# Kernel tuning notes

Hardware: AMD Instinct MI355X
Metric: run time of the kernel (lower is better)

Reference implementation:

```python
import jax, jax.numpy as jnp
import numpy as np

B, N = 4, 2048
INPUT_DIM, KDIM, VDIM = 128, 128, 16
EMBED, V_EMBED, H = 128, 128, 8
HEAD_DIM = EMBED // H          # 16
V_HEAD_DIM = V_EMBED // H      # 16 (== VDIM, required by the torch view)
SCALING = HEAD_DIM ** -0.5


def setup_inputs() -> dict:
    key = jax.random.key(0)
    ks = jax.random.split(key, 12)
    inp = {
        "query": jax.random.normal(ks[0], (B, N, INPUT_DIM), dtype=jnp.float32),
        "key": jax.random.normal(ks[1], (B, N, KDIM), dtype=jnp.float32),
        "value": jax.random.normal(ks[2], (B, N, VDIM), dtype=jnp.float32),
        # nn.Linear weights are [out, in]; init.normal_ -> std normal
        "Wq": jax.random.normal(ks[3], (EMBED, INPUT_DIM), dtype=jnp.float32),
        "bq": jnp.zeros((EMBED,), dtype=jnp.float32),
        "Wk": jax.random.normal(ks[4], (EMBED, KDIM), dtype=jnp.float32),
        "bk": jnp.zeros((EMBED,), dtype=jnp.float32),
        "Wv": jax.random.normal(ks[5], (V_EMBED, VDIM), dtype=jnp.float32),
        "bv": jnp.zeros((V_EMBED,), dtype=jnp.float32),
        "Wo": jax.random.normal(ks[6], (V_EMBED // H, V_EMBED), dtype=jnp.float32),
        "bo": jnp.zeros((V_EMBED // H,), dtype=jnp.float32),
    }
    return inp


def reference(query, key, value, Wq, bq, Wk, bk, Wv, bv, Wo, bo):
    # projections
    q = (query @ Wq.T + bq) * SCALING                 # [B, N, EMBED]
    k = key @ Wk.T + bk                               # [B, N, EMBED]
    v = value @ Wv.T + bv                             # [B, N, V_EMBED]
    # split heads: [B, H, N, head_dim]
    q = q.reshape(B, N, H, HEAD_DIM).transpose(0, 2, 1, 3)
    k = k.reshape(B, N, H, HEAD_DIM).transpose(0, 2, 1, 3)
    v = v.reshape(B, N, H, V_HEAD_DIM).transpose(0, 2, 1, 3)
    # full NxN scores (naive attention, as in the source)
    scores = jnp.einsum("bhnd,bhmd->bhnm", q, k)      # [B, H, N, N]
    attn = jax.nn.softmax(scores, axis=-1)
    # dropout is identity in eval mode
    ctx = jnp.einsum("bhnm,bhme->bhne", attn, v)      # [B, H, N, V_HEAD_DIM]
    ctx = ctx.transpose(0, 2, 1, 3).reshape(B, N, V_EMBED)
    out = ctx @ Wo.T + bo                             # [B, N, V_EMBED // H]
    return out
```

## Files before the change

kernel.cpp:

```cpp
#include <hip/hip_runtime.h>
#include <math.h>

typedef unsigned short ushort_t;
typedef unsigned int uint_t;
typedef __bf16 bf16x8 __attribute__((ext_vector_type(8)));
typedef float f32x4 __attribute__((ext_vector_type(4)));

#define NSEQ 2048
#define BH   32
#define QSCALE 0.3606737602222409f

__device__ __forceinline__ float exp2_fast(float x) {
#if __has_builtin(__builtin_amdgcn_exp2f)
    return __builtin_amdgcn_exp2f(x);
#else
    return exp2f(x);
#endif
}

__device__ __forceinline__ ushort_t f2bf(float x) {
    uint_t u = __float_as_uint(x);
    u += 0x7FFFu + ((u >> 16) & 1u);
    return (ushort_t)(u >> 16);
}
__device__ __forceinline__ float bf2f(ushort_t h) {
    return __uint_as_float(((uint_t)h) << 16);
}
__device__ __forceinline__ uint_t pkbf(float a, float b) {
    return ((__float_as_uint(a) + 0x8000u) >> 16) |
           ((__float_as_uint(b) + 0x8000u) & 0xFFFF0000u);
}

union U8 { ushort_t u[8]; bf16x8 v; uint4 q; };
union F8 { float f[8]; float4 v4[2]; };

__global__ __launch_bounds__(256) void wpack_kernel(
    const float* __restrict__ Wq, const float* __restrict__ Wk,
    ushort_t* __restrict__ wpk_hi, ushort_t* __restrict__ wpk_lo)
{
    const int idx  = blockIdx.x * 256 + threadIdx.x;
    const int lane = idx & 63;
    const int f    = (idx >> 6) & 3;
    const int ct   = (idx >> 8) & 7;
    const int mat  = idx >> 11;
    const float* W = mat ? Wk : Wq;
    const float* src = W + (size_t)(ct * 16 + (lane & 15)) * 128
                         + f * 32 + (lane >> 4) * 8;
    F8 x; x.v4[0] = *(const float4*)src; x.v4[1] = *(const float4*)(src + 4);
    U8 hi, lo;
#pragma unroll
    for (int j = 0; j < 8; ++j) {
        const ushort_t h = f2bf(x.f[j]);
        hi.u[j] = h;
        lo.u[j] = f2bf(x.f[j] - bf2f(h));
    }
    const size_t dst = (size_t)mat * 16384 + ((size_t)(ct * 4 + f) * 64 + lane) * 8;
    *(uint4*)(wpk_hi + dst) = hi.q;
    *(uint4*)(wpk_lo + dst) = lo.q;
}

__global__ __launch_bounds__(256, 2) void proj_kernel(
    const float* __restrict__ query, const float* __restrict__ key,
    const float* __restrict__ value,
    const float* __restrict__ bq, const float* __restrict__ bk,
    const float* __restrict__ Wv, const float* __restrict__ bv,
    const ushort_t* __restrict__ wpk_hi, const ushort_t* __restrict__ wpk_lo,
    ushort_t* __restrict__ q_hi, ushort_t* __restrict__ q_lo,
    ushort_t* __restrict__ k_hi, ushort_t* __restrict__ k_lo,
    ushort_t* __restrict__ vt)
{
    const int t   = threadIdx.x;
    const int w   = t >> 6;
    const int l   = t & 63;
    const int n16 = l & 15;
    const int g   = l >> 4;
    const int rbase = blockIdx.x * 16;
    const int b = rbase >> 11;

    const int isK    = w >> 1;
    const int cthalf = (w & 1) * 4;

    const float* X = isK ? key : query;
    const float* xrow = X + (size_t)(rbase + n16) * 128 + g * 8;
    bf16x8 ah[4], al[4];
#pragma unroll
    for (int f = 0; f < 4; ++f) {
        F8 x;
        x.v4[0] = *(const float4*)(xrow + f * 32);
        x.v4[1] = *(const float4*)(xrow + f * 32 + 4);
        U8 hi, lo;
#pragma unroll
        for (int j = 0; j < 8; ++j) {
            const ushort_t h = f2bf(x.f[j]);
            hi.u[j] = h;
            lo.u[j] = f2bf(x.f[j] - bf2f(h));
        }
        ah[f] = hi.v; al[f] = lo.v;
    }

    bf16x8 bhfr[4][4], blfr[4][4];
#pragma unroll
    for (int ctl = 0; ctl < 4; ++ctl) {
#pragma unroll
        for (int f = 0; f < 4; ++f) {
            const size_t o = (size_t)isK * 16384
                           + ((size_t)((cthalf + ctl) * 4 + f) * 64 + l) * 8;
            bhfr[ctl][f] = *(const bf16x8*)(wpk_hi + o);
            blfr[ctl][f] = *(const bf16x8*)(wpk_lo + o);
        }
    }

    const float* bias = isK ? bk : bq;
    ushort_t* dhi = isK ? k_hi : q_hi;
    ushort_t* dlo = isK ? k_lo : q_lo;
    const float scale = isK ? 1.0f : QSCALE;
    const int nbase = (rbase & 2047) + g * 4;

#pragma unroll
    for (int ctl = 0; ctl < 4; ++ctl) {
        const int h = cthalf + ctl;
        const float bval = bias[h * 16 + n16];
        f32x4 acc = {bval, bval, bval, bval};
#pragma unroll
        for (int f = 0; f < 4; ++f) {
            acc = __builtin_amdgcn_mfma_f32_16x16x32_bf16(ah[f], bhfr[ctl][f], acc, 0, 0, 0);
            acc = __builtin_amdgcn_mfma_f32_16x16x32_bf16(al[f], bhfr[ctl][f], acc, 0, 0, 0);
            acc = __builtin_amdgcn_mfma_f32_16x16x32_bf16(ah[f], blfr[ctl][f], acc, 0, 0, 0);
        }
        const size_t abase = ((size_t)(b * 8 + h) * NSEQ + nbase) * 16 + n16;
#pragma unroll
        for (int r = 0; r < 3 + 1; ++r) {
            const float vq = acc[r] * scale;
            const ushort_t hh = f2bf(vq);
            dhi[abase + (size_t)r * 16] = hh;
            dlo[abase + (size_t)r * 16] = f2bf(vq - bf2f(hh));
        }
    }

    const int e  = t & 127;
    const int rh = t >> 7;
    const int r0 = rbase + rh * 8;
    const float4* Wv4 = (const float4*)(Wv + (size_t)e * 16);
    const float4 wv0 = Wv4[0], wv1 = Wv4[1], wv2 = Wv4[2], wv3 = Wv4[3];
    const float bvv = bv[e];
    U8 vpk;
#pragma unroll
    for (int r = 0; r < 8; ++r) {
        const float4* xv4 = (const float4*)(value + (size_t)(r0 + r) * 16);
        const float4 x0 = xv4[0], x1 = xv4[1], x2 = xv4[2], x3 = xv4[3];
        float a = bvv;
        a += wv0.x*x0.x + wv0.y*x0.y + wv0.z*x0.z + wv0.w*x0.w;
        a += wv1.x*x1.x + wv1.y*x1.y + wv1.z*x1.z + wv1.w*x1.w;
        a += wv2.x*x2.x + wv2.y*x2.y + wv2.z*x2.z + wv2.w*x2.w;
        a += wv3.x*x3.x + wv3.y*x3.y + wv3.z*x3.z + wv3.w*x3.w;
        vpk.u[r] = f2bf(a);
    }
    const int hv = e >> 4, dd = e & 15;
    *(uint4*)(vt + ((size_t)(b * 8 + hv) * 16 + dd) * NSEQ + (r0 & 2047)) = vpk.q;
}

__global__ __launch_bounds__(256) void attn_kernel(
    const ushort_t* __restrict__ q_hi, const ushort_t* __restrict__ q_lo,
    const ushort_t* __restrict__ k_hi, const ushort_t* __restrict__ k_lo,
    const ushort_t* __restrict__ vt, float* __restrict__ ctx)
{
    const int t    = threadIdx.x;
    const int wave = t >> 6;
    const int l    = t & 63;
    const int col  = l & 15;
    const int g    = l >> 4;

    const int bh = blockIdx.y;
    const int qb = blockIdx.x * 64 + wave * 16;

    __shared__ __align__(16) ushort_t lds_p[4][16 * 40];
    ushort_t* pbuf = lds_p[wave];

    U8 Uz, Uo;
#pragma unroll
    for (int i = 0; i < 8; ++i) { Uz.u[i] = 0; Uo.u[i] = 0x3F80; }
    const bf16x8 zf = Uz.v, ones = Uo.v;

    const size_t qoff = ((size_t)(bh * NSEQ + qb + col)) * 16 + (g & 1) * 8;
    const bf16x8 bq1 = *(const bf16x8*)(q_hi + qoff);
    bf16x8 bq2 = *(const bf16x8*)(q_lo + qoff);
    bq2 = (g < 2) ? bq2 : zf;

    const ushort_t* ksel = (g < 2) ? k_hi : k_lo;
    const ushort_t* aptr = ksel + ((size_t)(bh * NSEQ + col)) * 16 + (g & 1) * 8;
    const ushort_t* vptr = vt + ((size_t)(bh * 16 + col)) * NSEQ + g * 8;

    f32x4 o    = {0.f, 0.f, 0.f, 0.f};
    f32x4 lacc = {0.f, 0.f, 0.f, 0.f};
    float m_run = -INFINITY;

    bf16x8 a1 = *(const bf16x8*)(aptr);
    bf16x8 a2 = *(const bf16x8*)(aptr + 256);
    bf16x8 av = *(const bf16x8*)(vptr);

    for (int kb = 0; kb < 64; ++kb) {
        const int kn = (kb + 1) & 63;
        bf16x8 na1 = *(const bf16x8*)(aptr + (size_t)kn * 512);
        bf16x8 na2 = *(const bf16x8*)(aptr + (size_t)kn * 512 + 256);
        bf16x8 nav = *(const bf16x8*)(vptr + (size_t)kn * 32);

        f32x4 z = {0.f, 0.f, 0.f, 0.f};
        f32x4 st1 = __builtin_amdgcn_mfma_f32_16x16x32_bf16(a1, bq2, z, 0, 0, 0);
        st1       = __builtin_amdgcn_mfma_f32_16x16x32_bf16(a1, bq1, st1, 0, 0, 0);
        f32x4 st2 = __builtin_amdgcn_mfma_f32_16x16x32_bf16(a2, bq2, z, 0, 0, 0);
        st2       = __builtin_amdgcn_mfma_f32_16x16x32_bf16(a2, bq1, st2, 0, 0, 0);

        float tm = fmaxf(fmaxf(fmaxf(st1[0], st1[1]), fmaxf(st1[2], st1[3])),
                         fmaxf(fmaxf(st2[0], st2[1]), fmaxf(st2[2], st2[3])));
        tm = fmaxf(tm, __shfl_xor(tm, 16));
        tm = fmaxf(tm, __shfl_xor(tm, 32));

        const float m_new = fmaxf(m_run, tm);
        const float alpha = exp2_fast(m_run - m_new);
        m_run = m_new;

        float p0 = exp2_fast(st1[0] - m_new);
        float p1 = exp2_fast(st1[1] - m_new);
        float p2 = exp2_fast(st1[2] - m_new);
        float p3 = exp2_fast(st1[3] - m_new);
        float p4 = exp2_fast(st2[0] - m_new);
        float p5 = exp2_fast(st2[1] - m_new);
        float p6 = exp2_fast(st2[2] - m_new);
        float p7 = exp2_fast(st2[3] - m_new);

        o[0] *= alpha; o[1] *= alpha; o[2] *= alpha; o[3] *= alpha;
        lacc[0] *= alpha; lacc[1] *= alpha; lacc[2] *= alpha; lacc[3] *= alpha;

        uint2 w1; w1.x = pkbf(p0, p1); w1.y = pkbf(p2, p3);
        uint2 w2; w2.x = pkbf(p4, p5); w2.y = pkbf(p6, p7);
        *(uint2*)(pbuf + col * 40 + 4 * g)      = w1;
        *(uint2*)(pbuf + col * 40 + 16 + 4 * g) = w2;
        const bf16x8 bp = *(const bf16x8*)(pbuf + col * 40 + 8 * g);

        o    = __builtin_amdgcn_mfma_f32_16x16x32_bf16(av,   bp, o,    0, 0, 0);
        lacc = __builtin_amdgcn_mfma_f32_16x16x32_bf16(ones, bp, lacc, 0, 0, 0);

        a1 = na1; a2 = na2; av = nav;
    }

    const float linv = 1.0f / lacc[0];
    f32x4 res;
    res[0] = o[0] * linv; res[1] = o[1] * linv;
    res[2] = o[2] * linv; res[3] = o[3] * linv;
    *(f32x4*)(ctx + ((size_t)(bh * NSEQ + qb + col)) * 16 + 4 * g) = res;
}

__global__ __launch_bounds__(256) void outproj_kernel(
    const float* __restrict__ ctxws, const float* __restrict__ Wo,
    const float* __restrict__ bo, float* __restrict__ out)
{
    __shared__ float wo_s[16 * 132];
    const int t = threadIdx.x;
    for (int i = t; i < 2048; i += 256) {
        const int j = i >> 7, e2 = i & 127;
        wo_s[j * 132 + e2] = Wo[i];
    }
    __syncthreads();

    const int rl = t >> 4, j = t & 15;
    const int row = blockIdx.x * 16 + rl;
    const int b = row >> 11, n = row & 2047;
    float acc = bo[j];
#pragma unroll
    for (int h = 0; h < 8; ++h) {
        const float4* cp4 = (const float4*)(ctxws + (((size_t)(b*8 + h) * NSEQ) + n) * 16);
#pragma unroll
        for (int d4 = 0; d4 < 4; ++d4) {
            const float4 cc = cp4[d4];
            const float* wp = &wo_s[j * 132 + h * 16 + d4 * 4];
            acc += cc.x*wp[0] + cc.y*wp[1] + cc.z*wp[2] + cc.w*wp[3];
        }
    }
    out[(size_t)row * 16 + j] = acc;
}

extern "C" void kernel_launch(void* const* d_in, const int* in_sizes, int n_in,
                              void* d_out, int out_size, void* d_ws, size_t ws_size,
                              hipStream_t stream)
{
    const float* query = (const float*)d_in[0];
    const float* key_  = (const float*)d_in[1];
    const float* value = (const float*)d_in[2];
    const float* Wq = (const float*)d_in[3];
    const float* bq = (const float*)d_in[4];
    const float* Wk = (const float*)d_in[5];
    const float* bk = (const float*)d_in[6];
    const float* Wv = (const float*)d_in[7];
    const float* bv = (const float*)d_in[8];
    const float* Wo = (const float*)d_in[9];
    const float* bo = (const float*)d_in[10];
    float* out = (float*)d_out;

    ushort_t* q_hi = (ushort_t*)d_ws;
    ushort_t* q_lo = q_hi + (1u << 20);
    ushort_t* k_hi = q_hi + (2u << 20);
    ushort_t* k_lo = q_hi + (3u << 20);
    ushort_t* vt   = q_hi + (4u << 20);
    float*    ctx  = (float*)((char*)d_ws + (10u << 20));
    ushort_t* wpk_hi = (ushort_t*)((char*)d_ws + (14u << 20));
    ushort_t* wpk_lo = wpk_hi + 32768;

    wpack_kernel<<<dim3(16), dim3(256), 0, stream>>>(Wq, Wk, wpk_hi, wpk_lo);
    proj_kernel<<<dim3(512), dim3(256), 0, stream>>>(
        query, key_, value, bq, bk, Wv, bv, wpk_hi, wpk_lo,
        q_hi, q_lo, k_hi, k_lo, vt);
    attn_kernel<<<dim3(32, 32), dim3(256), 0, stream>>>(
        q_hi, q_lo, k_hi, k_lo, vt, ctx);
    outproj_kernel<<<dim3(512), dim3(256), 0, stream>>>(ctx, Wo, bo, out);
}
```

Baseline: 146.3 us.

## Precompute row max in separate pass to drop online softmax rescaling

Adds a maxk_kernel that computes an approximate per-query row max (hi-only Q times K hi+lo) in a first pass. The attention kernel then folds -max into the MFMA accumulator init, which removes the per-block max reduction, the cross-lane shuffles and the alpha rescaling of the output and normalizer. Float-to-bf16 packing also switches to the packed hardware conversion intrinsic, and the projection weight fragments are loaded per iteration to lower register pressure. The cost is an extra full pass over K plus a kernel launch, and an approximate max that could allow slight overflow or underflow risk.

```diff
diff --git a/kernel.cpp b/kernel.cpp
--- a/kernel.cpp
+++ b/kernel.cpp
@@ -1,4 +1,5 @@
 #include <hip/hip_runtime.h>
+#include <hip/hip_bf16.h>
 #include <math.h>
 
 typedef unsigned short ushort_t;
@@ -18,21 +19,25 @@
 #endif
 }
 
-__device__ __forceinline__ ushort_t f2bf(float x) {
-    uint_t u = __float_as_uint(x);
-    u += 0x7FFFu + ((u >> 16) & 1u);
-    return (ushort_t)(u >> 16);
-}
-__device__ __forceinline__ float bf2f(ushort_t h) {
-    return __uint_as_float(((uint_t)h) << 16);
-}
-__device__ __forceinline__ uint_t pkbf(float a, float b) {
-    return ((__float_as_uint(a) + 0x8000u) >> 16) |
-           ((__float_as_uint(b) + 0x8000u) & 0xFFFF0000u);
-}
-
-union U8 { ushort_t u[8]; bf16x8 v; uint4 q; };
+union U8 { ushort_t u[8]; bf16x8 v; uint4 q; uint_t w[4]; };
 union F8 { float f[8]; float4 v4[2]; };
+
+__device__ __forceinline__ uint_t pk2(float a, float b) {
+    __hip_bfloat162 h2 = __float22bfloat162_rn(make_float2(a, b));
+    union { __hip_bfloat162 h; uint_t u; } cv; cv.h = h2; return cv.u;
+}
+
+__device__ __forceinline__ void split8(const F8& x, U8& hi, U8& lo) {
+#pragma unroll
+    for (int p = 0; p < 4; ++p) {
+        const float a = x.f[2*p], b = x.f[2*p+1];
+        const uint_t hw = pk2(a, b);
+        hi.w[p] = hw;
+        const float ha = __uint_as_float(hw << 16);
+        const float hb = __uint_as_float(hw & 0xFFFF0000u);
+        lo.w[p] = pk2(a - ha, b - hb);
+    }
+}
 
 __global__ __launch_bounds__(256) void wpack_kernel(
     const float* __restrict__ Wq, const float* __restrict__ Wk,
@@ -48,12 +53,7 @@
                          + f * 32 + (lane >> 4) * 8;
     F8 x; x.v4[0] = *(const float4*)src; x.v4[1] = *(const float4*)(src + 4);
     U8 hi, lo;
-#pragma unroll
-    for (int j = 0; j < 8; ++j) {
-        const ushort_t h = f2bf(x.f[j]);
-        hi.u[j] = h;
-        lo.u[j] = f2bf(x.f[j] - bf2f(h));
-    }
+    split8(x, hi, lo);
     const size_t dst = (size_t)mat * 16384 + ((size_t)(ct * 4 + f) * 64 + lane) * 8;
     *(uint4*)(wpk_hi + dst) = hi.q;
     *(uint4*)(wpk_lo + dst) = lo.q;
@@ -89,25 +89,8 @@
         x.v4[0] = *(const float4*)(xrow + f * 32);
         x.v4[1] = *(const float4*)(xrow + f * 32 + 4);
         U8 hi, lo;
-#pragma unroll
-        for (int j = 0; j < 8; ++j) {
-            const ushort_t h = f2bf(x.f[j]);
-            hi.u[j] = h;
-            lo.u[j] = f2bf(x.f[j] - bf2f(h));
-        }
+        split8(x, hi, lo);
         ah[f] = hi.v; al[f] = lo.v;
-    }
-
-    bf16x8 bhfr[4][4], blfr[4][4];
-#pragma unroll
-    for (int ctl = 0; ctl < 4; ++ctl) {
-#pragma unroll
-        for (int f = 0; f < 4; ++f) {
-            const size_t o = (size_t)isK * 16384
-                           + ((size_t)((cthalf + ctl) * 4 + f) * 64 + l) * 8;
-            bhfr[ctl][f] = *(const bf16x8*)(wpk_hi + o);
-            blfr[ctl][f] = *(const bf16x8*)(wpk_lo + o);
-        }
     }
 
     const float* bias = isK ? bk : bq;
@@ -116,25 +99,41 @@
     const float scale = isK ? 1.0f : QSCALE;
     const int nbase = (rbase & 2047) + g * 4;
 
-#pragma unroll
+#pragma unroll 1
     for (int ctl = 0; ctl < 4; ++ctl) {
         const int h = cthalf + ctl;
+        bf16x8 bhf[4], blf[4];
+#pragma unroll
+        for (int f = 0; f < 4; ++f) {
+            const size_t o = (size_t)isK * 16384
+                           + ((size_t)(h * 4 + f) * 64 + l) * 8;
+            bhf[f] = *(const bf16x8*)(wpk_hi + o);
+            blf[f] = *(const bf16x8*)(wpk_lo + o);
+        }
         const float bval = bias[h * 16 + n16];
         f32x4 acc = {bval, bval, bval, bval};
 #pragma unroll
         for (int f = 0; f < 4; ++f) {
-            acc = __builtin_amdgcn_mfma_f32_16x16x32_bf16(ah[f], bhfr[ctl][f], acc, 0, 0, 0);
-            acc = __builtin_amdgcn_mfma_f32_16x16x32_bf16(al[f], bhfr[ctl][f], acc, 0, 0, 0);
-            acc = __builtin_amdgcn_mfma_f32_16x16x32_bf16(ah[f], blfr[ctl][f], acc, 0, 0, 0);
+            acc = __builtin_amdgcn_mfma_f32_16x16x32_bf16(ah[f], bhf[f], acc, 0, 0, 0);
+            acc = __builtin_amdgcn_mfma_f32_16x16x32_bf16(al[f], bhf[f], acc, 0, 0, 0);
+            acc = __builtin_amdgcn_mfma_f32_16x16x32_bf16(ah[f], blf[f], acc, 0, 0, 0);
         }
         const size_t abase = ((size_t)(b * 8 + h) * NSEQ + nbase) * 16 + n16;
-#pragma unroll
-        for (int r = 0; r < 3 + 1; ++r) {
-            const float vq = acc[r] * scale;
-            const ushort_t hh = f2bf(vq);
-            dhi[abase + (size_t)r * 16] = hh;
-            dlo[abase + (size_t)r * 16] = f2bf(vq - bf2f(hh));
-        }
+        const float a0 = acc[0]*scale, a1 = acc[1]*scale;
+        const float a2 = acc[2]*scale, a3 = acc[3]*scale;
+        const uint_t h01 = pk2(a0, a1), h23 = pk2(a2, a3);
+        const uint_t l01 = pk2(a0 - __uint_as_float(h01 << 16),
+                               a1 - __uint_as_float(h01 & 0xFFFF0000u));
+        const uint_t l23 = pk2(a2 - __uint_as_float(h23 << 16),
+                               a3 - __uint_as_float(h23 & 0xFFFF0000u));
+        dhi[abase]      = (ushort_t)h01;
+        dhi[abase + 16] = (ushort_t)(h01 >> 16);
+        dhi[abase + 32] = (ushort_t)h23;
+        dhi[abase + 48] = (ushort_t)(h23 >> 16);
+        dlo[abase]      = (ushort_t)l01;
+        dlo[abase + 16] = (ushort_t)(l01 >> 16);
+        dlo[abase + 32] = (ushort_t)l23;
+        dlo[abase + 48] = (ushort_t)(l23 >> 16);
     }
 
     const int e  = t & 127;
@@ -143,7 +142,7 @@
     const float4* Wv4 = (const float4*)(Wv + (size_t)e * 16);
     const float4 wv0 = Wv4[0], wv1 = Wv4[1], wv2 = Wv4[2], wv3 = Wv4[3];
     const float bvv = bv[e];
-    U8 vpk;
+    F8 af;
 #pragma unroll
     for (int r = 0; r < 8; ++r) {
         const float4* xv4 = (const float4*)(value + (size_t)(r0 + r) * 16);
@@ -153,16 +152,19 @@
         a += wv1.x*x1.x + wv1.y*x1.y + wv1.z*x1.z + wv1.w*x1.w;
         a += wv2.x*x2.x + wv2.y*x2.y + wv2.z*x2.z + wv2.w*x2.w;
         a += wv3.x*x3.x + wv3.y*x3.y + wv3.z*x3.z + wv3.w*x3.w;
-        vpk.u[r] = f2bf(a);
-    }
+        af.f[r] = a;
+    }
+    U8 vpk;
+#pragma unroll
+    for (int p = 0; p < 4; ++p) vpk.w[p] = pk2(af.f[2*p], af.f[2*p+1]);
     const int hv = e >> 4, dd = e & 15;
     *(uint4*)(vt + ((size_t)(b * 8 + hv) * 16 + dd) * NSEQ + (r0 & 2047)) = vpk.q;
 }
 
-__global__ __launch_bounds__(256) void attn_kernel(
-    const ushort_t* __restrict__ q_hi, const ushort_t* __restrict__ q_lo,
+__global__ __launch_bounds__(256, 2) void maxk_kernel(
+    const ushort_t* __restrict__ q_hi,
     const ushort_t* __restrict__ k_hi, const ushort_t* __restrict__ k_lo,
-    const ushort_t* __restrict__ vt, float* __restrict__ ctx)
+    float* __restrict__ m_arr)
 {
     const int t    = threadIdx.x;
     const int wave = t >> 6;
@@ -173,6 +175,43 @@
     const int bh = blockIdx.y;
     const int qb = blockIdx.x * 64 + wave * 16;
 
+    const size_t qoff = ((size_t)(bh * NSEQ + qb + col)) * 16 + (g & 1) * 8;
+    const bf16x8 bq1 = *(const bf16x8*)(q_hi + qoff);
+
+    const ushort_t* ksel = (g < 2) ? k_hi : k_lo;
+    const ushort_t* aptr = ksel + ((size_t)(bh * NSEQ + col)) * 16 + (g & 1) * 8;
+
+    float mrun = -INFINITY;
+    const f32x4 z = {0.f, 0.f, 0.f, 0.f};
+#pragma unroll 2
+    for (int kb = 0; kb < 64; ++kb) {
+        const bf16x8 a1 = *(const bf16x8*)(aptr + (size_t)kb * 512);
+        const bf16x8 a2 = *(const bf16x8*)(aptr + (size_t)kb * 512 + 256);
+        const f32x4 st1 = __builtin_amdgcn_mfma_f32_16x16x32_bf16(a1, bq1, z, 0, 0, 0);
+        const f32x4 st2 = __builtin_amdgcn_mfma_f32_16x16x32_bf16(a2, bq1, z, 0, 0, 0);
+        mrun = fmaxf(mrun, fmaxf(fmaxf(st1[0], st1[1]), fmaxf(st1[2], st1[3])));
+        mrun = fmaxf(mrun, fmaxf(fmaxf(st2[0], st2[1]), fmaxf(st2[2], st2[3])));
+    }
+    mrun = fmaxf(mrun, __shfl_xor(mrun, 16));
+    mrun = fmaxf(mrun, __shfl_xor(mrun, 32));
+    if (l < 16) m_arr[bh * NSEQ + qb + col] = mrun;
+}
+
+__global__ __launch_bounds__(256, 2) void attn_kernel(
+    const ushort_t* __restrict__ q_hi, const ushort_t* __restrict__ q_lo,
+    const ushort_t* __restrict__ k_hi, const ushort_t* __restrict__ k_lo,
+    const ushort_t* __restrict__ vt, const float* __restrict__ m_arr,
+    float* __restrict__ ctx)
+{
+    const int t    = threadIdx.x;
+    const int wave = t >> 6;
+    const int l    = t & 63;
+    const int col  = l & 15;
+    const int g    = l >> 4;
+
+    const int bh = blockIdx.y;
+    const int qb = blockIdx.x * 64 + wave * 16;
+
     __shared__ __align__(16) ushort_t lds_p[4][16 * 40];
     ushort_t* pbuf = lds_p[wave];
 
@@ -186,13 +225,15 @@
     bf16x8 bq2 = *(const bf16x8*)(q_lo + qoff);
     bq2 = (g < 2) ? bq2 : zf;
 
+    const float mcol = m_arr[bh * NSEQ + qb + col];
+    const f32x4 zin = {-mcol, -mcol, -mcol, -mcol};
+
     const ushort_t* ksel = (g < 2) ? k_hi : k_lo;
     const ushort_t* aptr = ksel + ((size_t)(bh * NSEQ + col)) * 16 + (g & 1) * 8;
     const ushort_t* vptr = vt + ((size_t)(bh * 16 + col)) * NSEQ + g * 8;
 
     f32x4 o    = {0.f, 0.f, 0.f, 0.f};
     f32x4 lacc = {0.f, 0.f, 0.f, 0.f};
-    float m_run = -INFINITY;
 
     bf16x8 a1 = *(const bf16x8*)(aptr);
     bf16x8 a2 = *(const bf16x8*)(aptr + 256);
@@ -204,35 +245,22 @@
         bf16x8 na2 = *(const bf16x8*)(aptr + (size_t)kn * 512 + 256);
         bf16x8 nav = *(const bf16x8*)(vptr + (size_t)kn * 32);
 
-        f32x4 z = {0.f, 0.f, 0.f, 0.f};
-        f32x4 st1 = __builtin_amdgcn_mfma_f32_16x16x32_bf16(a1, bq2, z, 0, 0, 0);
+        f32x4 st1 = __builtin_amdgcn_mfma_f32_16x16x32_bf16(a1, bq2, zin, 0, 0, 0);
         st1       = __builtin_amdgcn_mfma_f32_16x16x32_bf16(a1, bq1, st1, 0, 0, 0);
-        f32x4 st2 = __builtin_amdgcn_mfma_f32_16x16x32_bf16(a2, bq2, z, 0, 0, 0);
+        f32x4 st2 = __builtin_amdgcn_mfma_f32_16x16x32_bf16(a2, bq2, zin, 0, 0, 0);
         st2       = __builtin_amdgcn_mfma_f32_16x16x32_bf16(a2, bq1, st2, 0, 0, 0);
 
-        float tm = fmaxf(fmaxf(fmaxf(st1[0], st1[1]), fmaxf(st1[2], st1[3])),
-                         fmaxf(fmaxf(st2[0], st2[1]), fmaxf(st2[2], st2[3])));
-        tm = fmaxf(tm, __shfl_xor(tm, 16));
-        tm = fmaxf(tm, __shfl_xor(tm, 32));
-
-        const float m_new = fmaxf(m_run, tm);
-        const float alpha = exp2_fast(m_run - m_new);
-        m_run = m_new;
-
-        float p0 = exp2_fast(st1[0] - m_new);
-        float p1 = exp2_fast(st1[1] - m_new);
-        float p2 = exp2_fast(st1[2] - m_new);
-        float p3 = exp2_fast(st1[3] - m_new);
-        float p4 = exp2_fast(st2[0] - m_new);
-        float p5 = exp2_fast(st2[1] - m_new);
-        float p6 = exp2_fast(st2[2] - m_new);
-        float p7 = exp2_fast(st2[3] - m_new);
-
-        o[0] *= alpha; o[1] *= alpha; o[2] *= alpha; o[3] *= alpha;
-        lacc[0] *= alpha; lacc[1] *= alpha; lacc[2] *= alpha; lacc[3] *= alpha;
-
-        uint2 w1; w1.x = pkbf(p0, p1); w1.y = pkbf(p2, p3);
-        uint2 w2; w2.x = pkbf(p4, p5); w2.y = pkbf(p6, p7);
+        const float p0 = exp2_fast(st1[0]);
+        const float p1 = exp2_fast(st1[1]);
+        const float p2 = exp2_fast(st1[2]);
+        const float p3 = exp2_fast(st1[3]);
+        const float p4 = exp2_fast(st2[0]);
+        const float p5 = exp2_fast(st2[1]);
+        const float p6 = exp2_fast(st2[2]);
+        const float p7 = exp2_fast(st2[3]);
+
+        uint2 w1; w1.x = pk2(p0, p1); w1.y = pk2(p2, p3);
+        uint2 w2; w2.x = pk2(p4, p5); w2.y = pk2(p6, p7);
         *(uint2*)(pbuf + col * 40 + 4 * g)      = w1;
         *(uint2*)(pbuf + col * 40 + 16 + 4 * g) = w2;
         const bf16x8 bp = *(const bf16x8*)(pbuf + col * 40 + 8 * g);
@@ -304,12 +332,14 @@
     float*    ctx  = (float*)((char*)d_ws + (10u << 20));
     ushort_t* wpk_hi = (ushort_t*)((char*)d_ws + (14u << 20));
     ushort_t* wpk_lo = wpk_hi + 32768;
+    float*    m_arr  = (float*)((char*)d_ws + (14u << 20) + (1u << 18));
 
     wpack_kernel<<<dim3(16), dim3(256), 0, stream>>>(Wq, Wk, wpk_hi, wpk_lo);
     proj_kernel<<<dim3(512), dim3(256), 0, stream>>>(
         query, key_, value, bq, bk, Wv, bv, wpk_hi, wpk_lo,
         q_hi, q_lo, k_hi, k_lo, vt);
+    maxk_kernel<<<dim3(32, 32), dim3(256), 0, stream>>>(q_hi, k_hi, k_lo, m_arr);
     attn_kernel<<<dim3(32, 32), dim3(256), 0, stream>>>(
-        q_hi, q_lo, k_hi, k_lo, vt, ctx);
+        q_hi, q_lo, k_hi, k_lo, vt, m_arr, ctx);
     outproj_kernel<<<dim3(512), dim3(256), 0, stream>>>(ctx, Wo, bo, out);
 }
```

New measurement: 158.5 us. 8.4% more time.
